# Performance work log

Measured on AMD Instinct MI355X. Metric: run time of the kernel, lower is better.

## Reference

```python
import jax, jax.numpy as jnp
import numpy as np

THRESHOLD = 0.5
NEG_POS_RATIO = 3
ALPHA = 10.0
N_PRIORS = 8732
N_CLASSES = 21
BATCH = 128
N_OBJ = 32


def cxcy_to_xy(cxcy):
    return jnp.concatenate([cxcy[..., :2] - cxcy[..., 2:] / 2.0,
                            cxcy[..., :2] + cxcy[..., 2:] / 2.0], axis=-1)


def xy_to_cxcy(xy):
    return jnp.concatenate([(xy[..., :2] + xy[..., 2:]) / 2.0,
                            xy[..., 2:] - xy[..., :2]], axis=-1)


def cxcy_to_gcxgcy(cxcy, priors_cxcy):
    return jnp.concatenate([(cxcy[..., :2] - priors_cxcy[..., :2]) / (priors_cxcy[..., 2:] / 10.0),
                            jnp.log(cxcy[..., 2:] / priors_cxcy[..., 2:]) * 5.0], axis=-1)


def find_jaccard_overlap(a, b):
    # a: (M,4) xyxy, b: (P,4) xyxy -> (M,P)
    lt = jnp.maximum(a[:, None, :2], b[None, :, :2])
    rb = jnp.minimum(a[:, None, 2:], b[None, :, 2:])
    wh = jnp.clip(rb - lt, 0.0)
    inter = wh[..., 0] * wh[..., 1]
    area_a = (a[:, 2] - a[:, 0]) * (a[:, 3] - a[:, 1])
    area_b = (b[:, 2] - b[:, 0]) * (b[:, 3] - b[:, 1])
    return inter / (area_a[:, None] + area_b[None, :] - inter)


def _match_one(boxes, labels, priors_xy, priors_cxcy):
    # boxes: (M,4) xyxy, labels: (M,)
    iou = find_jaccard_overlap(boxes, priors_xy)           # (M,P)
    obj_idx = jnp.argmax(iou, axis=1)                      # best prior per object
    iou = iou.at[jnp.arange(boxes.shape[0]), obj_idx].set(1.0)
    positive = (iou >= THRESHOLD).any(axis=0)              # (P,)
    max_prior_idx = jnp.argmax(iou, axis=0)                # best object per prior
    true_cls = labels[max_prior_idx] * positive.astype(labels.dtype)
    matched = boxes[max_prior_idx]                         # (P,4)
    true_locs = cxcy_to_gcxgcy(xy_to_cxcy(matched), priors_cxcy)
    return true_locs, true_cls, positive


def setup_inputs() -> dict:
    key = jax.random.key(0)
    k1, k2, k3, k4, k5, k6 = jax.random.split(key, 6)
    pred_loc = jax.random.normal(k1, (BATCH, N_PRIORS, 4), dtype=jnp.float32)
    pred_cls = jax.random.normal(k2, (BATCH, N_PRIORS, N_CLASSES), dtype=jnp.float32)
    # valid xyxy gt boxes in [0,1]
    p1 = jax.random.uniform(k3, (BATCH, N_OBJ, 2))
    p2 = jax.random.uniform(k4, (BATCH, N_OBJ, 2))
    b_boxes = jnp.concatenate([jnp.minimum(p1, p2), jnp.maximum(p1, p2) + 1e-3], axis=-1)
    b_boxes = jnp.clip(b_boxes, 0.0, 1.0).astype(jnp.float32)
    b_labels = jax.random.randint(k5, (BATCH, N_OBJ), 1, N_CLASSES)
    cxy = jax.random.uniform(k6, (N_PRIORS, 2), minval=0.1, maxval=0.9)
    wh = jax.random.uniform(jax.random.fold_in(k6, 1), (N_PRIORS, 2), minval=0.05, maxval=0.3)
    priors_cxcy = jnp.concatenate([cxy, wh], axis=-1).astype(jnp.float32)
    return {"pred_loc": pred_loc, "pred_cls": pred_cls, "b_boxes": b_boxes,
            "b_labels": b_labels, "priors_cxcy": priors_cxcy}


def reference(pred_loc, pred_cls, b_boxes, b_labels, priors_cxcy):
    batch_size, n_priors, n_classes = pred_cls.shape
    priors_xy = cxcy_to_xy(priors_cxcy)
    true_locs, true_classes, positive = jax.vmap(
        _match_one, in_axes=(0, 0, None, None))(b_boxes, b_labels, priors_xy, priors_cxcy)
    pos_f = positive.astype(pred_loc.dtype)                 # (B,P)
    n_positives = positive.sum(axis=1)                      # (B,)
    n_pos_total = n_positives.sum().astype(pred_loc.dtype)
    # L1 loss (mean over positive box elements)
    loc_loss = (jnp.abs(pred_loc - true_locs) * pos_f[..., None]).sum() / (n_pos_total * 4.0)
    # per-prior cross-entropy
    logp = jax.nn.log_softmax(pred_cls, axis=-1)
    ce = -jnp.take_along_axis(logp, true_classes[..., None], axis=-1)[..., 0]  # (B,P)
    conf_loss_pos = (ce * pos_f).sum()
    # hard negative mining: sort negatives descending per image
    conf_neg = jnp.where(positive, 0.0, ce)
    conf_neg_sorted = -jnp.sort(-conf_neg, axis=1)
    ranks = jnp.arange(n_priors)[None, :]
    hard_mask = ranks < (NEG_POS_RATIO * n_positives)[:, None]
    conf_loss_hard_neg = jnp.where(hard_mask, conf_neg_sorted, 0.0).sum()
    conf_loss = (conf_loss_hard_neg + conf_loss_pos) / n_pos_total
    loc_loss = ALPHA * loc_loss
    total_loss = conf_loss + loc_loss
    return total_loss, loc_loss, conf_loss
```

## Files before the change

### kernel.cpp

```cpp
#include <hip/hip_runtime.h>
#include <math.h>

#define B 128
#define M 32
#define P 8732
#define C 21
#define ALPHA 10.0f
#define TPB2 256
#define PPB 256
#define NB2 35
#define CH 8
#define CS 1092

#define GLD16(g, l)                                                   \
  __builtin_amdgcn_global_load_lds(                                   \
      (__attribute__((address_space(1))) void*)(g),                   \
      (__attribute__((address_space(3))) void*)(l), 16, 0, 0)

__global__ __launch_bounds__(256) void k1_partial(
    const float* __restrict__ b_boxes, const float* __restrict__ priors,
    float* __restrict__ pI, float* __restrict__ pU, int* __restrict__ pidx,
    int* __restrict__ done) {
  if (blockIdx.x == 0 && threadIdx.x == 0) *done = 0;
  int b = blockIdx.x >> 3;
  int ch = blockIdx.x & 7;
  int wid = threadIdx.x >> 6;
  int lane = threadIdx.x & 63;
  int obase = wid * 8;

  float ox1[8], oy1[8], ox2[8], oy2[8], oarea[8], bI[8], bU[8];
  int bidx[8];
#pragma unroll
  for (int k = 0; k < 8; k++) {
    float4 bx = ((const float4*)b_boxes)[(size_t)b * M + obase + k];
    ox1[k] = bx.x; oy1[k] = bx.y; ox2[k] = bx.z; oy2[k] = bx.w;
    oarea[k] = (bx.z - bx.x) * (bx.w - bx.y);
    bI[k] = -1.0f; bU[k] = 1.0f; bidx[k] = P;
  }

  int pend = (ch + 1) * CS;
  if (pend > P) pend = P;
#pragma unroll 2
  for (int p = ch * CS + lane; p < pend; p += 64) {
    float4 pr = ((const float4*)priors)[p];
    float pw2 = pr.z * 0.5f, ph2 = pr.w * 0.5f;
    float px1 = pr.x - pw2, py1 = pr.y - ph2;
    float px2 = pr.x + pw2, py2 = pr.y + ph2;
    float areaP = pr.z * pr.w;
#pragma unroll
    for (int k = 0; k < 8; k++) {
      float iw = fminf(ox2[k], px2) - fmaxf(ox1[k], px1);
      float ih = fminf(oy2[k], py2) - fmaxf(oy1[k], py1);
      iw = fmaxf(iw, 0.0f);
      ih = fmaxf(ih, 0.0f);
      float inter = iw * ih;
      float uni = oarea[k] + areaP - inter;
      if (inter * bU[k] > bI[k] * uni) { bI[k] = inter; bU[k] = uni; bidx[k] = p; }
    }
  }
  for (int off = 32; off >= 1; off >>= 1) {
#pragma unroll
    for (int k = 0; k < 8; k++) {
      float oI = __shfl_xor(bI[k], off, 64);
      float oU = __shfl_xor(bU[k], off, 64);
      int oi = __shfl_xor(bidx[k], off, 64);
      float l = oI * bU[k], r = bI[k] * oU;
      if (l > r || (l == r && oi < bidx[k])) { bI[k] = oI; bU[k] = oU; bidx[k] = oi; }
    }
  }
  if (lane == 0) {
#pragma unroll
    for (int k = 0; k < 8; k++) {
      int idx = ((size_t)b * M + obase + k) * CH + ch;
      pI[idx] = bI[k]; pU[idx] = bU[k]; pidx[idx] = bidx[k];
    }
  }
}

__global__ __launch_bounds__(TPB2) void k2_perprior(
    const float* __restrict__ pred_loc, const float* __restrict__ pred_cls,
    const float* __restrict__ b_boxes, const int* __restrict__ b_labels,
    const float* __restrict__ priors,
    const float* __restrict__ pI, const float* __restrict__ pU,
    const int* __restrict__ pidx,
    float* __restrict__ ploc, float* __restrict__ pce, int* __restrict__ pnp,
    float* __restrict__ confneg) {
  int b = blockIdx.y;
  int p0 = blockIdx.x * PPB;
  int tid = threadIdx.x;
  int wid = tid >> 6;
  int lane = tid & 63;

  __shared__ __align__(16) float sCls[4][64 * C];
  __shared__ __align__(16) float4 sbox[M];
  __shared__ float sarea[M];
  __shared__ int slab[M], sobj[M];
  __shared__ int sinv[PPB];

  {
    int wp0 = p0 + wid * 64;
    int nv = P - wp0;
    nv = nv < 0 ? 0 : (nv > 64 ? 64 : nv);
    int nf4 = (nv * C) >> 2;
    const float4* src = (const float4*)(pred_cls + ((size_t)b * P + wp0) * C);
#pragma unroll
    for (int k = 0; k < 6; k++) {
      int idx = (k << 6) + lane;
      if (idx < nf4) GLD16(src + idx, &sCls[wid][k << 8]);
    }
  }

  sinv[tid] = 0x7fffffff;
  if (tid < M) {
    int m = tid;
    float4 bx = ((const float4*)b_boxes)[b * M + m];
    sbox[m] = bx;
    sarea[m] = (bx.z - bx.x) * (bx.w - bx.y);
    slab[m] = b_labels[b * M + m];
    int o = b * M + m;
    float cI = pI[o * CH], cU = pU[o * CH];
    int ci = pidx[o * CH];
#pragma unroll
    for (int ch = 1; ch < CH; ch++) {
      float nI = pI[o * CH + ch], nU = pU[o * CH + ch];
      int ni = pidx[o * CH + ch];
      if (nI * cU > cI * nU) { cI = nI; cU = nU; ci = ni; }
    }
    sobj[m] = ci;
  }
  __syncthreads();
  if (tid < M) {
    int t = sobj[tid] - p0;
    if (t >= 0 && t < PPB) atomicMin(&sinv[t], tid);
  }
  __syncthreads();

  float locpart = 0.0f, cepospart = 0.0f;
  int npos = 0;
  int p = p0 + tid;
  if (p < P) {
    float4 pr = ((const float4*)priors)[p];
    float pw2 = pr.z * 0.5f, ph2 = pr.w * 0.5f;
    float px1 = pr.x - pw2, py1 = pr.y - ph2;
    float px2 = pr.x + pw2, py2 = pr.y + ph2;
    float areaP = pr.z * pr.w;
    float bI = -1.0f, bU = 1.0f;
    int bm = 0;
    for (int m = 0; m < M; m++) {
      float4 bx = sbox[m];
      float iw = fminf(bx.z, px2) - fmaxf(bx.x, px1);
      float ih = fminf(bx.w, py2) - fmaxf(bx.y, py1);
      iw = fmaxf(iw, 0.0f);
      ih = fmaxf(ih, 0.0f);
      float inter = iw * ih;
      float uni = sarea[m] + areaP - inter;
      if (inter * bU > bI * uni) { bI = inter; bU = uni; bm = m; }
    }
    int fm = sinv[tid];
    if (fm != 0x7fffffff) {
      if (!((bI == bU) && (bm < fm))) { bI = 1.0f; bU = 1.0f; bm = fm; }
    }
    bool pos = (2.0f * bI >= bU);
    int wAny = __any((int)pos);

    if (wAny) {
      float4 pl = ((const float4*)pred_loc)[(size_t)b * P + p];
      float4 bx = sbox[bm];
      float cx = (bx.x + bx.z) * 0.5f, cy = (bx.y + bx.w) * 0.5f;
      float w = bx.z - bx.x, h = bx.w - bx.y;
      float rz = __builtin_amdgcn_rcpf(pr.z);
      float rw = __builtin_amdgcn_rcpf(pr.w);
      float g0 = (cx - pr.x) * 10.0f * rz;
      float g1 = (cy - pr.y) * 10.0f * rw;
      float g2 = __logf(w * rz) * 5.0f;
      float g3 = __logf(h * rw) * 5.0f;
      if (pos) {
        locpart = fabsf(pl.x - g0) + fabsf(pl.y - g1) +
                  fabsf(pl.z - g2) + fabsf(pl.w - g3);
        npos = 1;
      }
    }

    const float* u = &sCls[wid][lane * C];
    int cls = pos ? slab[bm] : 0;
    float se = 0.0f, vc = 0.0f;
#pragma unroll
    for (int c = 0; c < C; c++) {
      float x = u[c];
      se += __expf(x);
      if (c == cls) vc = x;
    }
    float ce = __logf(se) - vc;
    confneg[(size_t)b * P + p] = pos ? 0.0f : ce;
    cepospart = pos ? ce : 0.0f;
  }

  for (int off = 32; off >= 1; off >>= 1) {
    locpart += __shfl_down(locpart, off, 64);
    cepospart += __shfl_down(cepospart, off, 64);
    npos += __shfl_down(npos, off, 64);
  }
  __shared__ float rloc[4], rce[4];
  __shared__ int rnp[4];
  if (lane == 0) { rloc[wid] = locpart; rce[wid] = cepospart; rnp[wid] = npos; }
  __syncthreads();
  if (tid == 0) {
    int f = b * NB2 + blockIdx.x;
    ploc[f] = rloc[0] + rloc[1] + rloc[2] + rloc[3];
    pce[f] = rce[0] + rce[1] + rce[2] + rce[3];
    pnp[f] = rnp[0] + rnp[1] + rnp[2] + rnp[3];
  }
}

__global__ __launch_bounds__(1024) void k3_hardneg(
    const float* __restrict__ confneg,
    const float* __restrict__ ploc, const float* __restrict__ pce,
    const int* __restrict__ pnp,
    float* __restrict__ imgres, int* __restrict__ done,
    float* __restrict__ out) {
  int b = blockIdx.x;
  int tid = threadIdx.x;
  int wid = tid >> 6;
  int lane = tid & 63;

  __shared__ __align__(16) float s[P];
  __shared__ int histw[16 * 256];
  __shared__ __align__(16) int cnt[256];
  __shared__ int sdig, scum, sK, sLast;
  __shared__ float sLoc, sCe, sNp;
  __shared__ float rsum[16], rl[16], rc[16], rh[16], rn[16];
  __shared__ int rcnt[16];

  {
    const float4* row4 = (const float4*)(confneg + (size_t)b * P);
    for (int i = tid; i < P / 4; i += 1024) ((float4*)s)[i] = row4[i];
  }

  if (wid == 0) {
    float lp = 0.0f, cp = 0.0f;
    int np = 0;
    if (lane < NB2) {
      int f = b * NB2 + lane;
      lp = ploc[f]; cp = pce[f]; np = pnp[f];
    }
    for (int off = 32; off >= 1; off >>= 1) {
      lp += __shfl_down(lp, off, 64);
      cp += __shfl_down(cp, off, 64);
      np += __shfl_down(np, off, 64);
    }
    if (lane == 0) {
      int K = np * 3;
      if (K > P) K = P;
      sK = K; sLoc = lp; sCe = cp; sNp = (float)np;
    }
  }
  __syncthreads();

  int K = sK;
  unsigned pfx = 0;
  int Krem = K;
#pragma unroll
  for (int pass = 3; pass >= 0; --pass) {
    int sh = pass * 8;
    for (int i = tid; i < 16 * 256; i += 1024) histw[i] = 0;
    __syncthreads();
    unsigned himask = (pass == 3) ? 0u : (0xFFFFFFFFu << (sh + 8));
    int* myh = &histw[wid * 256];
    for (int i = tid; i < P; i += 1024) {
      unsigned ub = __float_as_uint(s[i]);
      if ((ub & himask) == pfx) atomicAdd(&myh[(ub >> sh) & 255], 1);
    }
    __syncthreads();
    if (tid < 256) {
      int c = 0;
#pragma unroll
      for (int w = 0; w < 16; w++) c += histw[w * 256 + tid];
      cnt[tid] = c;
    }
    __syncthreads();
    if (wid == 0) {
      int4 c4 = ((const int4*)cnt)[lane];
      int s3 = c4.w;
      int s2 = c4.z + s3;
      int s1 = c4.y + s2;
      int s0 = c4.x + s1;
      int suf = s0;
      for (int off = 1; off < 64; off <<= 1) {
        int t = __shfl_down(suf, off, 64);
        if (lane + off < 64) suf += t;
      }
      int above = suf - s0;
      int S0 = above + s0, S1 = above + s1, S2 = above + s2, S3 = above + s3;
      int S4 = above;
      if (S3 >= Krem && S4 < Krem) { sdig = 4 * lane + 3; scum = S4; }
      else if (S2 >= Krem && S3 < Krem) { sdig = 4 * lane + 2; scum = S3; }
      else if (S1 >= Krem && S2 < Krem) { sdig = 4 * lane + 1; scum = S2; }
      else if (S0 >= Krem && S1 < Krem) { sdig = 4 * lane + 0; scum = S1; }
    }
    __syncthreads();
    pfx |= ((unsigned)sdig) << sh;
    Krem -= scum;
  }
  float tau = __uint_as_float(pfx);

  float sum = 0.0f;
  int cgt = 0;
  for (int i = tid; i < P; i += 1024) {
    float v = s[i];
    if (v > tau) { sum += v; cgt++; }
  }
  for (int off = 32; off >= 1; off >>= 1) {
    sum += __shfl_down(sum, off, 64);
    cgt += __shfl_down(cgt, off, 64);
  }
  if (lane == 0) { rsum[wid] = sum; rcnt[wid] = cgt; }
  __syncthreads();
  if (tid == 0) {
    float stot = 0.0f;
    int ctot = 0;
#pragma unroll
    for (int w = 0; w < 16; w++) { stot += rsum[w]; ctot += rcnt[w]; }
    float hard = stot + (float)(K - ctot) * tau;
    imgres[b * 4 + 0] = sLoc;
    imgres[b * 4 + 1] = sCe;
    imgres[b * 4 + 2] = hard;
    imgres[b * 4 + 3] = sNp;
    __threadfence();
    int prev = atomicAdd(done, 1);
    sLast = (prev == B - 1) ? 1 : 0;
  }
  __syncthreads();
  if (sLast) {
    __threadfence();
    float l = 0.0f, c = 0.0f, h = 0.0f, n = 0.0f;
    if (tid < B) {
      l = atomicAdd(&imgres[tid * 4 + 0], 0.0f);
      c = atomicAdd(&imgres[tid * 4 + 1], 0.0f);
      h = atomicAdd(&imgres[tid * 4 + 2], 0.0f);
      n = atomicAdd(&imgres[tid * 4 + 3], 0.0f);
    }
    for (int off = 32; off >= 1; off >>= 1) {
      l += __shfl_down(l, off, 64);
      c += __shfl_down(c, off, 64);
      h += __shfl_down(h, off, 64);
      n += __shfl_down(n, off, 64);
    }
    if (lane == 0) { rl[wid] = l; rc[wid] = c; rh[wid] = h; rn[wid] = n; }
    __syncthreads();
    if (tid == 0) {
      float L = 0, Cc = 0, H = 0, N = 0;
#pragma unroll
      for (int w = 0; w < 16; w++) { L += rl[w]; Cc += rc[w]; H += rh[w]; N += rn[w]; }
      float loc = ALPHA * L / (N * 4.0f);
      float conf = (H + Cc) / N;
      out[0] = conf + loc;
      out[1] = loc;
      out[2] = conf;
    }
  }
}

extern "C" void kernel_launch(void* const* d_in, const int* in_sizes, int n_in,
                              void* d_out, int out_size, void* d_ws, size_t ws_size,
                              hipStream_t stream) {
  (void)in_sizes; (void)n_in; (void)out_size; (void)ws_size;
  const float* pred_loc = (const float*)d_in[0];
  const float* pred_cls = (const float*)d_in[1];
  const float* b_boxes = (const float*)d_in[2];
  const int* b_labels = (const int*)d_in[3];
  const float* priors = (const float*)d_in[4];
  float* out = (float*)d_out;

  int* done = (int*)d_ws;
  float* ploc = (float*)d_ws + 8;
  float* pce = ploc + B * NB2;
  int* pnp = (int*)(pce + B * NB2);
  float* imgres = (float*)(pnp + B * NB2);
  float* pI = imgres + B * 4;
  float* pU = pI + B * M * CH;
  int* pidx = (int*)(pU + B * M * CH);
  float* confneg = (float*)(pidx + B * M * CH);

  k1_partial<<<B * CH, 256, 0, stream>>>(b_boxes, priors, pI, pU, pidx, done);
  dim3 g2(NB2, B);
  k2_perprior<<<g2, TPB2, 0, stream>>>(pred_loc, pred_cls, b_boxes, b_labels,
                                       priors, pI, pU, pidx,
                                       ploc, pce, pnp, confneg);
  k3_hardneg<<<B, 1024, 0, stream>>>(confneg, ploc, pce, pnp, imgres, done, out);
}
```

Baseline: 214.5 us.

## Fuse per-prior and hard-negative kernels via last-block-per-image counter

Merges the per-prior loss kernel and the hard-negative radix-select kernel into one launch. The last of the 35 blocks per image, detected with an atomic counter, runs the radix select over that image's confneg row, now read from global/L2 with float4 loads instead of being staged in LDS, using 256 threads instead of 1024. Shared memory is reused through a union. This removes a kernel launch and lets selection for early-finishing images overlap with other blocks. The risk is that the serial selection tail runs on fewer threads and re-reads the row from cache four times.

Measured after the change: 504.6 us. 2.35x slower.

```diff
diff --git a/kernel.cpp b/kernel.cpp
--- a/kernel.cpp
+++ b/kernel.cpp
@@ -20,8 +20,11 @@
 __global__ __launch_bounds__(256) void k1_partial(
     const float* __restrict__ b_boxes, const float* __restrict__ priors,
     float* __restrict__ pI, float* __restrict__ pU, int* __restrict__ pidx,
-    int* __restrict__ done) {
-  if (blockIdx.x == 0 && threadIdx.x == 0) *done = 0;
+    int* __restrict__ done, int* __restrict__ imgcnt) {
+  if (blockIdx.x == 0) {
+    if (threadIdx.x == 0) *done = 0;
+    if (threadIdx.x < B) imgcnt[threadIdx.x] = 0;
+  }
   int b = blockIdx.x >> 3;
   int ch = blockIdx.x & 7;
   int wid = threadIdx.x >> 6;
@@ -77,25 +80,43 @@
   }
 }
 
-__global__ __launch_bounds__(TPB2) void k2_perprior(
+__global__ __launch_bounds__(TPB2) void k23_fused(
     const float* __restrict__ pred_loc, const float* __restrict__ pred_cls,
     const float* __restrict__ b_boxes, const int* __restrict__ b_labels,
     const float* __restrict__ priors,
     const float* __restrict__ pI, const float* __restrict__ pU,
     const int* __restrict__ pidx,
     float* __restrict__ ploc, float* __restrict__ pce, int* __restrict__ pnp,
-    float* __restrict__ confneg) {
+    float* __restrict__ confneg, int* __restrict__ imgcnt,
+    float* __restrict__ imgres, int* __restrict__ done,
+    float* __restrict__ out) {
   int b = blockIdx.y;
   int p0 = blockIdx.x * PPB;
   int tid = threadIdx.x;
   int wid = tid >> 6;
   int lane = tid & 63;
 
-  __shared__ __align__(16) float sCls[4][64 * C];
-  __shared__ __align__(16) float4 sbox[M];
-  __shared__ float sarea[M];
-  __shared__ int slab[M], sobj[M];
-  __shared__ int sinv[PPB];
+  __shared__ __align__(16) union SU {
+    struct {
+      float cls[4][64 * C];
+      float4 box[M];
+      float area[M];
+      int lab[M];
+      int obj[M];
+      int inv[PPB];
+    } a;
+    struct {
+      int histw[4 * 256];
+      int cnt[256];
+      float rsum[4];
+      int rcnt[4];
+      float rl[4], rc[4], rh[4], rn[4];
+    } s3;
+  } u;
+  __shared__ float rloc[4], rce[4];
+  __shared__ int rnp[4];
+  __shared__ int sdig, scum, sLastBlk, sLastImg, sK;
+  __shared__ float sLoc, sCe, sNp;
 
   {
     int wp0 = p0 + wid * 64;
@@ -106,17 +127,17 @@
 #pragma unroll
     for (int k = 0; k < 6; k++) {
       int idx = (k << 6) + lane;
-      if (idx < nf4) GLD16(src + idx, &sCls[wid][k << 8]);
-    }
-  }
-
-  sinv[tid] = 0x7fffffff;
+      if (idx < nf4) GLD16(src + idx, &u.a.cls[wid][k << 8]);
+    }
+  }
+
+  u.a.inv[tid] = 0x7fffffff;
   if (tid < M) {
     int m = tid;
     float4 bx = ((const float4*)b_boxes)[b * M + m];
-    sbox[m] = bx;
-    sarea[m] = (bx.z - bx.x) * (bx.w - bx.y);
-    slab[m] = b_labels[b * M + m];
+    u.a.box[m] = bx;
+    u.a.area[m] = (bx.z - bx.x) * (bx.w - bx.y);
+    u.a.lab[m] = b_labels[b * M + m];
     int o = b * M + m;
     float cI = pI[o * CH], cU = pU[o * CH];
     int ci = pidx[o * CH];
@@ -126,12 +147,12 @@
       int ni = pidx[o * CH + ch];
       if (nI * cU > cI * nU) { cI = nI; cU = nU; ci = ni; }
     }
-    sobj[m] = ci;
+    u.a.obj[m] = ci;
   }
   __syncthreads();
   if (tid < M) {
-    int t = sobj[tid] - p0;
-    if (t >= 0 && t < PPB) atomicMin(&sinv[t], tid);
+    int t = u.a.obj[tid] - p0;
+    if (t >= 0 && t < PPB) atomicMin(&u.a.inv[t], tid);
   }
   __syncthreads();
 
@@ -147,16 +168,16 @@
     float bI = -1.0f, bU = 1.0f;
     int bm = 0;
     for (int m = 0; m < M; m++) {
-      float4 bx = sbox[m];
+      float4 bx = u.a.box[m];
       float iw = fminf(bx.z, px2) - fmaxf(bx.x, px1);
       float ih = fminf(bx.w, py2) - fmaxf(bx.y, py1);
       iw = fmaxf(iw, 0.0f);
       ih = fmaxf(ih, 0.0f);
       float inter = iw * ih;
-      float uni = sarea[m] + areaP - inter;
+      float uni = u.a.area[m] + areaP - inter;
       if (inter * bU > bI * uni) { bI = inter; bU = uni; bm = m; }
     }
-    int fm = sinv[tid];
+    int fm = u.a.inv[tid];
     if (fm != 0x7fffffff) {
       if (!((bI == bU) && (bm < fm))) { bI = 1.0f; bU = 1.0f; bm = fm; }
     }
@@ -165,7 +186,7 @@
 
     if (wAny) {
       float4 pl = ((const float4*)pred_loc)[(size_t)b * P + p];
-      float4 bx = sbox[bm];
+      float4 bx = u.a.box[bm];
       float cx = (bx.x + bx.z) * 0.5f, cy = (bx.y + bx.w) * 0.5f;
       float w = bx.z - bx.x, h = bx.w - bx.y;
       float rz = __builtin_amdgcn_rcpf(pr.z);
@@ -181,12 +202,12 @@
       }
     }
 
-    const float* u = &sCls[wid][lane * C];
-    int cls = pos ? slab[bm] : 0;
+    const float* cptr = &u.a.cls[wid][lane * C];
+    int cls = pos ? u.a.lab[bm] : 0;
     float se = 0.0f, vc = 0.0f;
 #pragma unroll
     for (int c = 0; c < C; c++) {
-      float x = u[c];
+      float x = cptr[c];
       se += __expf(x);
       if (c == cls) vc = x;
     }
@@ -200,8 +221,6 @@
     cepospart += __shfl_down(cepospart, off, 64);
     npos += __shfl_down(npos, off, 64);
   }
-  __shared__ float rloc[4], rce[4];
-  __shared__ int rnp[4];
   if (lane == 0) { rloc[wid] = locpart; rce[wid] = cepospart; rnp[wid] = npos; }
   __syncthreads();
   if (tid == 0) {
@@ -209,32 +228,13 @@
     ploc[f] = rloc[0] + rloc[1] + rloc[2] + rloc[3];
     pce[f] = rce[0] + rce[1] + rce[2] + rce[3];
     pnp[f] = rnp[0] + rnp[1] + rnp[2] + rnp[3];
-  }
-}
-
-__global__ __launch_bounds__(1024) void k3_hardneg(
-    const float* __restrict__ confneg,
-    const float* __restrict__ ploc, const float* __restrict__ pce,
-    const int* __restrict__ pnp,
-    float* __restrict__ imgres, int* __restrict__ done,
-    float* __restrict__ out) {
-  int b = blockIdx.x;
-  int tid = threadIdx.x;
-  int wid = tid >> 6;
-  int lane = tid & 63;
-
-  __shared__ __align__(16) float s[P];
-  __shared__ int histw[16 * 256];
-  __shared__ __align__(16) int cnt[256];
-  __shared__ int sdig, scum, sK, sLast;
-  __shared__ float sLoc, sCe, sNp;
-  __shared__ float rsum[16], rl[16], rc[16], rh[16], rn[16];
-  __shared__ int rcnt[16];
-
-  {
-    const float4* row4 = (const float4*)(confneg + (size_t)b * P);
-    for (int i = tid; i < P / 4; i += 1024) ((float4*)s)[i] = row4[i];
-  }
+    __threadfence();
+    int prev = atomicAdd(&imgcnt[b], 1);
+    sLastBlk = (prev == NB2 - 1) ? 1 : 0;
+  }
+  __syncthreads();
+  if (!sLastBlk) return;
+  __threadfence();
 
   if (wid == 0) {
     float lp = 0.0f, cp = 0.0f;
@@ -256,32 +256,37 @@
   }
   __syncthreads();
 
+  const float4* row4 = (const float4*)(confneg + (size_t)b * P);
   int K = sK;
   unsigned pfx = 0;
   int Krem = K;
 #pragma unroll
   for (int pass = 3; pass >= 0; --pass) {
     int sh = pass * 8;
-    for (int i = tid; i < 16 * 256; i += 1024) histw[i] = 0;
+    for (int i = tid; i < 4 * 256; i += TPB2) u.s3.histw[i] = 0;
     __syncthreads();
     unsigned himask = (pass == 3) ? 0u : (0xFFFFFFFFu << (sh + 8));
-    int* myh = &histw[wid * 256];
-    for (int i = tid; i < P; i += 1024) {
-      unsigned ub = __float_as_uint(s[i]);
-      if ((ub & himask) == pfx) atomicAdd(&myh[(ub >> sh) & 255], 1);
-    }
-    __syncthreads();
-    if (tid < 256) {
-      int c = 0;
-#pragma unroll
-      for (int w = 0; w < 16; w++) c += histw[w * 256 + tid];
-      cnt[tid] = c;
+    int* myh = &u.s3.histw[wid * 256];
+    for (int i = tid; i < P / 4; i += TPB2) {
+      float4 v = row4[i];
+      unsigned u0 = __float_as_uint(v.x), u1 = __float_as_uint(v.y);
+      unsigned u2 = __float_as_uint(v.z), u3 = __float_as_uint(v.w);
+      if ((u0 & himask) == pfx) atomicAdd(&myh[(u0 >> sh) & 255], 1);
+      if ((u1 & himask) == pfx) atomicAdd(&myh[(u1 >> sh) & 255], 1);
+      if ((u2 & himask) == pfx) atomicAdd(&myh[(u2 >> sh) & 255], 1);
+      if ((u3 & himask) == pfx) atomicAdd(&myh[(u3 >> sh) & 255], 1);
+    }
+    __syncthreads();
+    {
+      int c = u.s3.histw[tid] + u.s3.histw[256 + tid] +
+              u.s3.histw[512 + tid] + u.s3.histw[768 + tid];
+      u.s3.cnt[tid] = c;
     }
     __syncthreads();
     if (wid == 0) {
-      int4 c4 = ((const int4*)cnt)[lane];
-      int s3 = c4.w;
-      int s2 = c4.z + s3;
+      int4 c4 = ((const int4*)u.s3.cnt)[lane];
+      int s3v = c4.w;
+      int s2 = c4.z + s3v;
       int s1 = c4.y + s2;
       int s0 = c4.x + s1;
       int suf = s0;
@@ -290,7 +295,7 @@
         if (lane + off < 64) suf += t;
       }
       int above = suf - s0;
-      int S0 = above + s0, S1 = above + s1, S2 = above + s2, S3 = above + s3;
+      int S0 = above + s0, S1 = above + s1, S2 = above + s2, S3 = above + s3v;
       int S4 = above;
       if (S3 >= Krem && S4 < Krem) { sdig = 4 * lane + 3; scum = S4; }
       else if (S2 >= Krem && S3 < Krem) { sdig = 4 * lane + 2; scum = S3; }
@@ -305,21 +310,22 @@
 
   float sum = 0.0f;
   int cgt = 0;
-  for (int i = tid; i < P; i += 1024) {
-    float v = s[i];
-    if (v > tau) { sum += v; cgt++; }
+  for (int i = tid; i < P / 4; i += TPB2) {
+    float4 v = row4[i];
+    if (v.x > tau) { sum += v.x; cgt++; }
+    if (v.y > tau) { sum += v.y; cgt++; }
+    if (v.z > tau) { sum += v.z; cgt++; }
+    if (v.w > tau) { sum += v.w; cgt++; }
   }
   for (int off = 32; off >= 1; off >>= 1) {
     sum += __shfl_down(sum, off, 64);
     cgt += __shfl_down(cgt, off, 64);
   }
-  if (lane == 0) { rsum[wid] = sum; rcnt[wid] = cgt; }
+  if (lane == 0) { u.s3.rsum[wid] = sum; u.s3.rcnt[wid] = cgt; }
   __syncthreads();
   if (tid == 0) {
-    float stot = 0.0f;
-    int ctot = 0;
-#pragma unroll
-    for (int w = 0; w < 16; w++) { stot += rsum[w]; ctot += rcnt[w]; }
+    float stot = u.s3.rsum[0] + u.s3.rsum[1] + u.s3.rsum[2] + u.s3.rsum[3];
+    int ctot = u.s3.rcnt[0] + u.s3.rcnt[1] + u.s3.rcnt[2] + u.s3.rcnt[3];
     float hard = stot + (float)(K - ctot) * tau;
     imgres[b * 4 + 0] = sLoc;
     imgres[b * 4 + 1] = sCe;
@@ -327,10 +333,10 @@
     imgres[b * 4 + 3] = sNp;
     __threadfence();
     int prev = atomicAdd(done, 1);
-    sLast = (prev == B - 1) ? 1 : 0;
-  }
-  __syncthreads();
-  if (sLast) {
+    sLastImg = (prev == B - 1) ? 1 : 0;
+  }
+  __syncthreads();
+  if (sLastImg) {
     __threadfence();
     float l = 0.0f, c = 0.0f, h = 0.0f, n = 0.0f;
     if (tid < B) {
@@ -345,12 +351,14 @@
       h += __shfl_down(h, off, 64);
       n += __shfl_down(n, off, 64);
     }
-    if (lane == 0) { rl[wid] = l; rc[wid] = c; rh[wid] = h; rn[wid] = n; }
+    if (lane == 0) { u.s3.rl[wid] = l; u.s3.rc[wid] = c; u.s3.rh[wid] = h; u.s3.rn[wid] = n; }
     __syncthreads();
     if (tid == 0) {
       float L = 0, Cc = 0, H = 0, N = 0;
 #pragma unroll
-      for (int w = 0; w < 16; w++) { L += rl[w]; Cc += rc[w]; H += rh[w]; N += rn[w]; }
+      for (int w = 0; w < 4; w++) {
+        L += u.s3.rl[w]; Cc += u.s3.rc[w]; H += u.s3.rh[w]; N += u.s3.rn[w];
+      }
       float loc = ALPHA * L / (N * 4.0f);
       float conf = (H + Cc) / N;
       out[0] = conf + loc;
@@ -372,7 +380,8 @@
   float* out = (float*)d_out;
 
   int* done = (int*)d_ws;
-  float* ploc = (float*)d_ws + 8;
+  int* imgcnt = (int*)d_ws + 8;
+  float* ploc = (float*)d_ws + 8 + B;
   float* pce = ploc + B * NB2;
   int* pnp = (int*)(pce + B * NB2);
   float* imgres = (float*)(pnp + B * NB2);
@@ -381,10 +390,9 @@
   int* pidx = (int*)(pU + B * M * CH);
   float* confneg = (float*)(pidx + B * M * CH);
 
-  k1_partial<<<B * CH, 256, 0, stream>>>(b_boxes, priors, pI, pU, pidx, done);
+  k1_partial<<<B * CH, 256, 0, stream>>>(b_boxes, priors, pI, pU, pidx, done, imgcnt);
   dim3 g2(NB2, B);
-  k2_perprior<<<g2, TPB2, 0, stream>>>(pred_loc, pred_cls, b_boxes, b_labels,
-                                       priors, pI, pU, pidx,
-                                       ploc, pce, pnp, confneg);
-  k3_hardneg<<<B, 1024, 0, stream>>>(confneg, ploc, pce, pnp, imgres, done, out);
+  k23_fused<<<g2, TPB2, 0, stream>>>(pred_loc, pred_cls, b_boxes, b_labels,
+                                     priors, pI, pU, pidx, ploc, pce, pnp,
+                                     confneg, imgcnt, imgres, done, out);
 }
```

## Fuse per-prior matching and hard-negative mining into one per-image kernel

Applied to the files above, without the earlier changes.

Merges the per-prior matching/cross-entropy kernel into the per-image hard-negative kernel, so confneg and the per-block partial sums stay in LDS instead of round-tripping through global memory. This removes one launch and the intermediate write and read. In exchange the grid shrinks to one block per image, which lowers parallelism. The class logits are now read directly from global memory with strided per-thread loads instead of coalesced async LDS staging, and the inverse best-prior lookup becomes a linear scan over objects.

Result: slower. 246.9 us (+15.1%).

```diff
diff --git a/kernel.cpp b/kernel.cpp
--- a/kernel.cpp
+++ b/kernel.cpp
@@ -6,16 +6,9 @@
 #define P 8732
 #define C 21
 #define ALPHA 10.0f
-#define TPB2 256
-#define PPB 256
 #define NB2 35
 #define CH 8
 #define CS 1092
-
-#define GLD16(g, l)                                                   \
-  __builtin_amdgcn_global_load_lds(                                   \
-      (__attribute__((address_space(1))) void*)(g),                   \
-      (__attribute__((address_space(3))) void*)(l), 16, 0, 0)
 
 __global__ __launch_bounds__(256) void k1_partial(
     const float* __restrict__ b_boxes, const float* __restrict__ priors,
@@ -77,40 +70,32 @@
   }
 }
 
-__global__ __launch_bounds__(TPB2) void k2_perprior(
+__global__ __launch_bounds__(1024) void k23_img(
     const float* __restrict__ pred_loc, const float* __restrict__ pred_cls,
     const float* __restrict__ b_boxes, const int* __restrict__ b_labels,
     const float* __restrict__ priors,
     const float* __restrict__ pI, const float* __restrict__ pU,
     const int* __restrict__ pidx,
-    float* __restrict__ ploc, float* __restrict__ pce, int* __restrict__ pnp,
-    float* __restrict__ confneg) {
-  int b = blockIdx.y;
-  int p0 = blockIdx.x * PPB;
+    float* __restrict__ imgres, int* __restrict__ done,
+    float* __restrict__ out) {
+  int b = blockIdx.x;
   int tid = threadIdx.x;
   int wid = tid >> 6;
   int lane = tid & 63;
 
-  __shared__ __align__(16) float sCls[4][64 * C];
+  __shared__ __align__(16) float s[P];
   __shared__ __align__(16) float4 sbox[M];
   __shared__ float sarea[M];
   __shared__ int slab[M], sobj[M];
-  __shared__ int sinv[PPB];
-
-  {
-    int wp0 = p0 + wid * 64;
-    int nv = P - wp0;
-    nv = nv < 0 ? 0 : (nv > 64 ? 64 : nv);
-    int nf4 = (nv * C) >> 2;
-    const float4* src = (const float4*)(pred_cls + ((size_t)b * P + wp0) * C);
-#pragma unroll
-    for (int k = 0; k < 6; k++) {
-      int idx = (k << 6) + lane;
-      if (idx < nf4) GLD16(src + idx, &sCls[wid][k << 8]);
-    }
-  }
-
-  sinv[tid] = 0x7fffffff;
+  __shared__ float pl[NB2], pc[NB2];
+  __shared__ int pn[NB2];
+  __shared__ int histw[16 * 256];
+  __shared__ __align__(16) int cnt[256];
+  __shared__ int sdig, scum, sK, sLast;
+  __shared__ float sLoc, sCe, sNp;
+  __shared__ float rsum[16], rl[16], rc[16], rh[16], rn[16];
+  __shared__ int rcnt[16];
+
   if (tid < M) {
     int m = tid;
     float4 bx = ((const float4*)b_boxes)[b * M + m];
@@ -129,120 +114,86 @@
     sobj[m] = ci;
   }
   __syncthreads();
-  if (tid < M) {
-    int t = sobj[tid] - p0;
-    if (t >= 0 && t < PPB) atomicMin(&sinv[t], tid);
-  }
-  __syncthreads();
-
-  float locpart = 0.0f, cepospart = 0.0f;
-  int npos = 0;
-  int p = p0 + tid;
-  if (p < P) {
-    float4 pr = ((const float4*)priors)[p];
-    float pw2 = pr.z * 0.5f, ph2 = pr.w * 0.5f;
-    float px1 = pr.x - pw2, py1 = pr.y - ph2;
-    float px2 = pr.x + pw2, py2 = pr.y + ph2;
-    float areaP = pr.z * pr.w;
-    float bI = -1.0f, bU = 1.0f;
-    int bm = 0;
-    for (int m = 0; m < M; m++) {
-      float4 bx = sbox[m];
-      float iw = fminf(bx.z, px2) - fmaxf(bx.x, px1);
-      float ih = fminf(bx.w, py2) - fmaxf(bx.y, py1);
-      iw = fmaxf(iw, 0.0f);
-      ih = fmaxf(ih, 0.0f);
-      float inter = iw * ih;
-      float uni = sarea[m] + areaP - inter;
-      if (inter * bU > bI * uni) { bI = inter; bU = uni; bm = m; }
-    }
-    int fm = sinv[tid];
-    if (fm != 0x7fffffff) {
-      if (!((bI == bU) && (bm < fm))) { bI = 1.0f; bU = 1.0f; bm = fm; }
-    }
-    bool pos = (2.0f * bI >= bU);
-    int wAny = __any((int)pos);
-
-    if (wAny) {
-      float4 pl = ((const float4*)pred_loc)[(size_t)b * P + p];
-      float4 bx = sbox[bm];
-      float cx = (bx.x + bx.z) * 0.5f, cy = (bx.y + bx.w) * 0.5f;
-      float w = bx.z - bx.x, h = bx.w - bx.y;
-      float rz = __builtin_amdgcn_rcpf(pr.z);
-      float rw = __builtin_amdgcn_rcpf(pr.w);
-      float g0 = (cx - pr.x) * 10.0f * rz;
-      float g1 = (cy - pr.y) * 10.0f * rw;
-      float g2 = __logf(w * rz) * 5.0f;
-      float g3 = __logf(h * rw) * 5.0f;
-      if (pos) {
-        locpart = fabsf(pl.x - g0) + fabsf(pl.y - g1) +
-                  fabsf(pl.z - g2) + fabsf(pl.w - g3);
-        npos = 1;
+
+  for (int x = wid; x < NB2; x += 16) {
+    float accl = 0.0f, accc = 0.0f;
+    int accn = 0;
+    for (int w4 = 0; w4 < 4; w4++) {
+      int p = x * 256 + w4 * 64 + lane;
+      float locpart = 0.0f, cepospart = 0.0f;
+      int npos = 0;
+      if (p < P) {
+        float4 pr = ((const float4*)priors)[p];
+        float pw2 = pr.z * 0.5f, ph2 = pr.w * 0.5f;
+        float px1 = pr.x - pw2, py1 = pr.y - ph2;
+        float px2 = pr.x + pw2, py2 = pr.y + ph2;
+        float areaP = pr.z * pr.w;
+        float bI = -1.0f, bU = 1.0f;
+        int bm = 0;
+        int fm = 0x7fffffff;
+        for (int m = 0; m < M; m++) {
+          float4 bx = sbox[m];
+          float iw = fminf(bx.z, px2) - fmaxf(bx.x, px1);
+          float ih = fminf(bx.w, py2) - fmaxf(bx.y, py1);
+          iw = fmaxf(iw, 0.0f);
+          ih = fmaxf(ih, 0.0f);
+          float inter = iw * ih;
+          float uni = sarea[m] + areaP - inter;
+          if (inter * bU > bI * uni) { bI = inter; bU = uni; bm = m; }
+          if (fm == 0x7fffffff && sobj[m] == p) fm = m;
+        }
+        if (fm != 0x7fffffff) {
+          if (!((bI == bU) && (bm < fm))) { bI = 1.0f; bU = 1.0f; bm = fm; }
+        }
+        bool pos = (2.0f * bI >= bU);
+        int wAny = __any((int)pos);
+
+        if (wAny) {
+          float4 plv = ((const float4*)pred_loc)[(size_t)b * P + p];
+          float4 bx = sbox[bm];
+          float cx = (bx.x + bx.z) * 0.5f, cy = (bx.y + bx.w) * 0.5f;
+          float w = bx.z - bx.x, h = bx.w - bx.y;
+          float rz = __builtin_amdgcn_rcpf(pr.z);
+          float rw = __builtin_amdgcn_rcpf(pr.w);
+          float g0 = (cx - pr.x) * 10.0f * rz;
+          float g1 = (cy - pr.y) * 10.0f * rw;
+          float g2 = __logf(w * rz) * 5.0f;
+          float g3 = __logf(h * rw) * 5.0f;
+          if (pos) {
+            locpart = fabsf(plv.x - g0) + fabsf(plv.y - g1) +
+                      fabsf(plv.z - g2) + fabsf(plv.w - g3);
+            npos = 1;
+          }
+        }
+
+        const float* uu = pred_cls + ((size_t)b * P + p) * C;
+        int cls = pos ? slab[bm] : 0;
+        float se = 0.0f, vc = 0.0f;
+#pragma unroll
+        for (int c = 0; c < C; c++) {
+          float xv = uu[c];
+          se += __expf(xv);
+          if (c == cls) vc = xv;
+        }
+        float ce = __logf(se) - vc;
+        s[p] = pos ? 0.0f : ce;
+        cepospart = pos ? ce : 0.0f;
       }
-    }
-
-    const float* u = &sCls[wid][lane * C];
-    int cls = pos ? slab[bm] : 0;
-    float se = 0.0f, vc = 0.0f;
-#pragma unroll
-    for (int c = 0; c < C; c++) {
-      float x = u[c];
-      se += __expf(x);
-      if (c == cls) vc = x;
-    }
-    float ce = __logf(se) - vc;
-    confneg[(size_t)b * P + p] = pos ? 0.0f : ce;
-    cepospart = pos ? ce : 0.0f;
-  }
-
-  for (int off = 32; off >= 1; off >>= 1) {
-    locpart += __shfl_down(locpart, off, 64);
-    cepospart += __shfl_down(cepospart, off, 64);
-    npos += __shfl_down(npos, off, 64);
-  }
-  __shared__ float rloc[4], rce[4];
-  __shared__ int rnp[4];
-  if (lane == 0) { rloc[wid] = locpart; rce[wid] = cepospart; rnp[wid] = npos; }
-  __syncthreads();
-  if (tid == 0) {
-    int f = b * NB2 + blockIdx.x;
-    ploc[f] = rloc[0] + rloc[1] + rloc[2] + rloc[3];
-    pce[f] = rce[0] + rce[1] + rce[2] + rce[3];
-    pnp[f] = rnp[0] + rnp[1] + rnp[2] + rnp[3];
-  }
-}
-
-__global__ __launch_bounds__(1024) void k3_hardneg(
-    const float* __restrict__ confneg,
-    const float* __restrict__ ploc, const float* __restrict__ pce,
-    const int* __restrict__ pnp,
-    float* __restrict__ imgres, int* __restrict__ done,
-    float* __restrict__ out) {
-  int b = blockIdx.x;
-  int tid = threadIdx.x;
-  int wid = tid >> 6;
-  int lane = tid & 63;
-
-  __shared__ __align__(16) float s[P];
-  __shared__ int histw[16 * 256];
-  __shared__ __align__(16) int cnt[256];
-  __shared__ int sdig, scum, sK, sLast;
-  __shared__ float sLoc, sCe, sNp;
-  __shared__ float rsum[16], rl[16], rc[16], rh[16], rn[16];
-  __shared__ int rcnt[16];
-
-  {
-    const float4* row4 = (const float4*)(confneg + (size_t)b * P);
-    for (int i = tid; i < P / 4; i += 1024) ((float4*)s)[i] = row4[i];
-  }
+      for (int off = 32; off >= 1; off >>= 1) {
+        locpart += __shfl_down(locpart, off, 64);
+        cepospart += __shfl_down(cepospart, off, 64);
+        npos += __shfl_down(npos, off, 64);
+      }
+      if (lane == 0) { accl += locpart; accc += cepospart; accn += npos; }
+    }
+    if (lane == 0) { pl[x] = accl; pc[x] = accc; pn[x] = accn; }
+  }
+  __syncthreads();
 
   if (wid == 0) {
     float lp = 0.0f, cp = 0.0f;
     int np = 0;
-    if (lane < NB2) {
-      int f = b * NB2 + lane;
-      lp = ploc[f]; cp = pce[f]; np = pnp[f];
-    }
+    if (lane < NB2) { lp = pl[lane]; cp = pc[lane]; np = pn[lane]; }
     for (int off = 32; off >= 1; off >>= 1) {
       lp += __shfl_down(lp, off, 64);
       cp += __shfl_down(cp, off, 64);
@@ -372,19 +323,12 @@
   float* out = (float*)d_out;
 
   int* done = (int*)d_ws;
-  float* ploc = (float*)d_ws + 8;
-  float* pce = ploc + B * NB2;
-  int* pnp = (int*)(pce + B * NB2);
-  float* imgres = (float*)(pnp + B * NB2);
+  float* imgres = (float*)d_ws + 8;
   float* pI = imgres + B * 4;
   float* pU = pI + B * M * CH;
   int* pidx = (int*)(pU + B * M * CH);
-  float* confneg = (float*)(pidx + B * M * CH);
 
   k1_partial<<<B * CH, 256, 0, stream>>>(b_boxes, priors, pI, pU, pidx, done);
-  dim3 g2(NB2, B);
-  k2_perprior<<<g2, TPB2, 0, stream>>>(pred_loc, pred_cls, b_boxes, b_labels,
-                                       priors, pI, pU, pidx,
-                                       ploc, pce, pnp, confneg);
-  k3_hardneg<<<B, 1024, 0, stream>>>(confneg, ploc, pce, pnp, imgres, done, out);
+  k23_img<<<B, 1024, 0, stream>>>(pred_loc, pred_cls, b_boxes, b_labels,
+                                  priors, pI, pU, pidx, imgres, done, out);
 }
```
